# Optimization experiments

Hardware: AMD Instinct MI355X
Metric: run time of the kernel (lower is better)

The kernel has to match this reference:

```python
import jax, jax.numpy as jnp
import numpy as np

N = 100000  # nodes
E = 1600000  # edges


def _gcn_norm(edge_index, num_nodes):
    # PyG GCNConv default: add self-loops, symmetric normalization.
    src, dst = edge_index[0], edge_index[1]
    loop = jnp.arange(num_nodes, dtype=src.dtype)
    src = jnp.concatenate([src, loop])
    dst = jnp.concatenate([dst, loop])
    deg = jax.ops.segment_sum(jnp.ones_like(dst, dtype=jnp.float32), dst,
                              num_segments=num_nodes)
    dinv = jnp.where(deg > 0, jax.lax.rsqrt(deg), 0.0)
    norm = dinv[src] * dinv[dst]  # [E + N]
    return src, dst, norm


def _gcn_layer(x, W, b, src, dst, norm, num_nodes):
    h = x @ W                                # [N, out]
    msg = h[src] * norm[:, None]             # gather + scale, [E+N, out]
    agg = jax.ops.segment_sum(msg, dst, num_segments=num_nodes)
    return agg + b


def setup_inputs() -> dict:
    key = jax.random.key(0)
    ks = jax.random.split(key, 8)
    d_in, d_h, d_out = 128, 128, 64
    x = jax.random.normal(ks[0], (N, d_in), dtype=jnp.float32)
    edge_index = jax.random.randint(ks[1], (2, E), 0, N, dtype=jnp.int64)
    def glorot(k, fan_in, fan_out):
        s = jnp.sqrt(6.0 / (fan_in + fan_out)).astype(jnp.float32)
        return jax.random.uniform(k, (fan_in, fan_out), jnp.float32, -s, s)
    return {
        "x": x,
        "edge_index": edge_index,
        "W1": glorot(ks[2], d_in, d_h), "b1": jnp.zeros((d_h,), jnp.float32),
        "W2": glorot(ks[3], d_h, d_h), "b2": jnp.zeros((d_h,), jnp.float32),
        "W3": glorot(ks[4], d_h, d_out), "b3": jnp.zeros((d_out,), jnp.float32),
    }


def reference(x, edge_index, W1, b1, W2, b2, W3, b3):
    src, dst, norm = _gcn_norm(edge_index, N)
    h = jax.nn.relu(_gcn_layer(x, W1, b1, src, dst, norm, N))
    h = jax.nn.relu(_gcn_layer(h, W2, b2, src, dst, norm, N))
    h = jax.nn.relu(_gcn_layer(h, W3, b3, src, dst, norm, N))
    return h
```

## Files before the change

### kernel.cpp

```cpp
#include <hip/hip_runtime.h>
#include <hip/hip_bf16.h>
#include <hip/hip_fp16.h>


constexpr int N_NODES = 100000;
constexpr int E_EDGES = 1600000;
constexpr int SCAN_B = (N_NODES + 1023) / 1024;

typedef short short8 __attribute__((ext_vector_type(8)));
typedef float f32x4 __attribute__((ext_vector_type(4)));

__global__ __launch_bounds__(256) void count_kernel(
    const int* __restrict__ dst, int* __restrict__ cnt) {
  int e = blockIdx.x * 256 + threadIdx.x;
  if (e < E_EDGES) atomicAdd(&cnt[dst[e]], 1);
}

__global__ __launch_bounds__(256) void scan_part_kernel(
    const int* __restrict__ cnt, int* __restrict__ bsum) {
  __shared__ int red[256];
  const int t = threadIdx.x;
  int base = blockIdx.x * 1024 + t * 4;
  int4 v = make_int4(0, 0, 0, 0);
  if (base < N_NODES) v = *(const int4*)(cnt + base);
  red[t] = v.x + v.y + v.z + v.w;
  __syncthreads();
  for (int off = 128; off > 0; off >>= 1) {
    if (t < off) red[t] += red[t + off];
    __syncthreads();
  }
  if (t == 0) bsum[blockIdx.x] = red[0];
}

__global__ __launch_bounds__(128) void scan_tops_kernel(
    const int* __restrict__ bsum, int* __restrict__ boff,
    int* __restrict__ rowptr) {
  __shared__ int part[128];
  const int t = threadIdx.x;
  int v = (t < SCAN_B) ? bsum[t] : 0;
  part[t] = v;
  __syncthreads();
  for (int off = 1; off < 128; off <<= 1) {
    int add = (t >= off) ? part[t - off] : 0;
    __syncthreads();
    part[t] += add;
    __syncthreads();
  }
  if (t < SCAN_B) boff[t] = part[t] - v;
  if (t == 127) rowptr[N_NODES] = part[127];
}

__global__ __launch_bounds__(256) void scan_write_kernel(
    const int* __restrict__ cnt, const int* __restrict__ boff,
    int* __restrict__ rowptr, float* __restrict__ dinv) {
  __shared__ int part[256];
  const int t = threadIdx.x;
  int base = blockIdx.x * 1024 + t * 4;
  int4 v = make_int4(0, 0, 0, 0);
  if (base < N_NODES) v = *(const int4*)(cnt + base);
  int s = v.x + v.y + v.z + v.w;
  part[t] = s;
  __syncthreads();
  for (int off = 1; off < 256; off <<= 1) {
    int add = (t >= off) ? part[t - off] : 0;
    __syncthreads();
    part[t] += add;
    __syncthreads();
  }
  if (base < N_NODES) {
    int run = boff[blockIdx.x] + part[t] - s;
    int4 o;
    o.x = run;
    o.y = run + v.x;
    o.z = run + v.x + v.y;
    o.w = run + v.x + v.y + v.z;
    *(int4*)(rowptr + base) = o;
    float4 dv;
    dv.x = rsqrtf((float)v.x + 1.0f);
    dv.y = rsqrtf((float)v.y + 1.0f);
    dv.z = rsqrtf((float)v.z + 1.0f);
    dv.w = rsqrtf((float)v.w + 1.0f);
    *(float4*)(dinv + base) = dv;
  }
}

__global__ __launch_bounds__(256) void scatter_kernel(
    const int* __restrict__ src, const int* __restrict__ dst,
    const int* __restrict__ rowptr, int* __restrict__ cursor,
    const float* __restrict__ dinv, int* __restrict__ eSrc,
    float* __restrict__ eW) {
  int e = blockIdx.x * 256 + threadIdx.x;
  if (e < E_EDGES) {
    int s = src[e], d = dst[e];
    int pos = rowptr[d] + atomicAdd(&cursor[d], 1);
    eSrc[pos] = s;
    eW[pos] = dinv[s] * dinv[d];
  }
}

__device__ inline ushort bf_round(float x) {
  uint u = __float_as_uint(x);
  return (ushort)((u + 0x7FFFu + ((u >> 16) & 1u)) >> 16);
}
__device__ inline ushort bf_split(float x, float* rem) {
  ushort h = bf_round(x);
  *rem = x - __uint_as_float((uint)h << 16);
  return h;
}

template <int OC>
__global__ __launch_bounds__(256) void packw_kernel(
    const float* __restrict__ W, ushort* __restrict__ hi,
    ushort* __restrict__ lo) {
  int id = blockIdx.x * 256 + threadIdx.x;
  if (id >= OC * 16) return;
  int col = id & 15;
  int g = (id >> 4) & 3;
  int ks = (id >> 6) & 3;
  int nt = id >> 8;
  int k0 = ks * 32 + g * 8;
  int n = nt * 16 + col;
  ushort h8[8], l8[8];
#pragma unroll
  for (int j = 0; j < 8; ++j) {
    float rem;
    h8[j] = bf_split(W[(size_t)(k0 + j) * OC + n], &rem);
    l8[j] = bf_round(rem);
  }
  size_t base = (size_t)id * 8;
#pragma unroll
  for (int j = 0; j < 8; ++j) {
    hi[base + j] = h8[j];
    lo[base + j] = l8[j];
  }
}

template <int OC>
__global__ __launch_bounds__(256) void gemm_kernel(
    const float* __restrict__ X, const ushort* __restrict__ Whi,
    const ushort* __restrict__ Wlo, __half* __restrict__ H) {
  constexpr int NT = OC / 16;
  __shared__ ushort sWhi[OC * 128];
  __shared__ ushort sWlo[OC * 128];
  const int t = threadIdx.x;
  {
    const uint4* gh = (const uint4*)Whi;
    const uint4* gl = (const uint4*)Wlo;
    uint4* sh = (uint4*)sWhi;
    uint4* sl = (uint4*)sWlo;
    for (int i = t; i < OC * 128 / 8; i += 256) {
      sh[i] = gh[i];
      sl[i] = gl[i];
    }
  }
  const int wid = t >> 6;
  const int lane = t & 63;
  const int row = blockIdx.x * 64 + wid * 16 + (lane & 15);
  const bool ok = row < N_NODES;
  const int g = lane >> 4;

  short8 ahi[4], alo[4];
  const float* xr = X + (size_t)row * 128;
#pragma unroll
  for (int ks = 0; ks < 4; ++ks) {
    float f[8];
    if (ok) {
      float4 f0 = *(const float4*)(xr + ks * 32 + g * 8);
      float4 f1 = *(const float4*)(xr + ks * 32 + g * 8 + 4);
      f[0] = f0.x; f[1] = f0.y; f[2] = f0.z; f[3] = f0.w;
      f[4] = f1.x; f[5] = f1.y; f[6] = f1.z; f[7] = f1.w;
    } else {
#pragma unroll
      for (int j = 0; j < 8; ++j) f[j] = 0.f;
    }
    union { short8 v; ushort u[8]; } h, l;
#pragma unroll
    for (int j = 0; j < 8; ++j) {
      float rem;
      h.u[j] = bf_split(f[j], &rem);
      l.u[j] = bf_round(rem);
    }
    ahi[ks] = h.v;
    alo[ks] = l.v;
  }
  __syncthreads();

#pragma unroll
  for (int nt = 0; nt < NT; ++nt) {
    f32x4 acc = {0.f, 0.f, 0.f, 0.f};
#pragma unroll
    for (int ks = 0; ks < 4; ++ks) {
      int off = (((nt * 4 + ks) * 4 + g) * 16 + (lane & 15)) * 8;
      short8 bhi = *(const short8*)&sWhi[off];
      short8 blo = *(const short8*)&sWlo[off];
      acc = __builtin_amdgcn_mfma_f32_16x16x32_bf16(alo[ks], bhi, acc, 0, 0, 0);
      acc = __builtin_amdgcn_mfma_f32_16x16x32_bf16(ahi[ks], blo, acc, 0, 0, 0);
      acc = __builtin_amdgcn_mfma_f32_16x16x32_bf16(ahi[ks], bhi, acc, 0, 0, 0);
    }
#pragma unroll
    for (int r = 0; r < 4; ++r) {
      int rr = blockIdx.x * 64 + wid * 16 + g * 4 + r;
      if (rr < N_NODES)
        H[(size_t)rr * OC + nt * 16 + (lane & 15)] = __float2half(acc[r]);
    }
  }
}

template <int OC>
__global__ __launch_bounds__(256) void agg_kernel(
    const __half* __restrict__ H, const int* __restrict__ rowptr,
    const int* __restrict__ eSrc, const float* __restrict__ eW,
    const float* __restrict__ dinv, const float* __restrict__ bias,
    float* __restrict__ Y) {
  const int wave = threadIdx.x >> 6;
  const int lane = threadIdx.x & 63;
  const int n = blockIdx.x * 4 + wave;
  if (n >= N_NODES) return;
  const float dn = dinv[n];
  const float selfw = dn * dn;
  const int beg = rowptr[n], end = rowptr[n + 1];
  const int jal = min((beg + 3) & ~3, end);
  const int jend = jal + ((end - jal) & ~7);
  const int jend4 = jend + ((end - jend) & ~3);

  if constexpr (OC == 128) {
    const __half2* H2 = (const __half2*)H;
    float2 hv = __half22float2(H2[(size_t)n * 64 + lane]);
    float ax = hv.x * selfw, ay = hv.y * selfw;
    for (int j = beg; j < jal; ++j) {
      float w = eW[j];
      float2 v = __half22float2(H2[(size_t)eSrc[j] * 64 + lane]);
      ax = fmaf(v.x, w, ax);
      ay = fmaf(v.y, w, ay);
    }
    for (int j = jal; j < jend; j += 8) {
      int4 s0 = *(const int4*)(eSrc + j);
      int4 s1 = *(const int4*)(eSrc + j + 4);
      float4 w0 = *(const float4*)(eW + j);
      float4 w1 = *(const float4*)(eW + j + 4);
      __half2 h0 = H2[(size_t)s0.x * 64 + lane];
      __half2 h1 = H2[(size_t)s0.y * 64 + lane];
      __half2 h2 = H2[(size_t)s0.z * 64 + lane];
      __half2 h3 = H2[(size_t)s0.w * 64 + lane];
      __half2 h4 = H2[(size_t)s1.x * 64 + lane];
      __half2 h5 = H2[(size_t)s1.y * 64 + lane];
      __half2 h6 = H2[(size_t)s1.z * 64 + lane];
      __half2 h7 = H2[(size_t)s1.w * 64 + lane];
      float2 v0 = __half22float2(h0);
      float2 v1 = __half22float2(h1);
      float2 v2 = __half22float2(h2);
      float2 v3 = __half22float2(h3);
      float2 v4 = __half22float2(h4);
      float2 v5 = __half22float2(h5);
      float2 v6 = __half22float2(h6);
      float2 v7 = __half22float2(h7);
      ax = fmaf(v0.x, w0.x, ax); ay = fmaf(v0.y, w0.x, ay);
      ax = fmaf(v1.x, w0.y, ax); ay = fmaf(v1.y, w0.y, ay);
      ax = fmaf(v2.x, w0.z, ax); ay = fmaf(v2.y, w0.z, ay);
      ax = fmaf(v3.x, w0.w, ax); ay = fmaf(v3.y, w0.w, ay);
      ax = fmaf(v4.x, w1.x, ax); ay = fmaf(v4.y, w1.x, ay);
      ax = fmaf(v5.x, w1.y, ax); ay = fmaf(v5.y, w1.y, ay);
      ax = fmaf(v6.x, w1.z, ax); ay = fmaf(v6.y, w1.z, ay);
      ax = fmaf(v7.x, w1.w, ax); ay = fmaf(v7.y, w1.w, ay);
    }
    for (int j = jend; j < jend4; j += 4) {
      int4 s = *(const int4*)(eSrc + j);
      float4 w = *(const float4*)(eW + j);
      float2 v0 = __half22float2(H2[(size_t)s.x * 64 + lane]);
      float2 v1 = __half22float2(H2[(size_t)s.y * 64 + lane]);
      float2 v2 = __half22float2(H2[(size_t)s.z * 64 + lane]);
      float2 v3 = __half22float2(H2[(size_t)s.w * 64 + lane]);
      ax = fmaf(v0.x, w.x, ax); ay = fmaf(v0.y, w.x, ay);
      ax = fmaf(v1.x, w.y, ax); ay = fmaf(v1.y, w.y, ay);
      ax = fmaf(v2.x, w.z, ax); ay = fmaf(v2.y, w.z, ay);
      ax = fmaf(v3.x, w.w, ax); ay = fmaf(v3.y, w.w, ay);
    }
    for (int j = jend4; j < end; ++j) {
      float w = eW[j];
      float2 v = __half22float2(H2[(size_t)eSrc[j] * 64 + lane]);
      ax = fmaf(v.x, w, ax);
      ay = fmaf(v.y, w, ay);
    }
    float2 bb = ((const float2*)bias)[lane];
    float2 o;
    o.x = fmaxf(ax + bb.x, 0.f);
    o.y = fmaxf(ay + bb.y, 0.f);
    ((float2*)Y)[(size_t)n * 64 + lane] = o;
  } else {
    float a = __half2float(H[(size_t)n * 64 + lane]) * selfw;
    for (int j = beg; j < jal; ++j)
      a = fmaf(__half2float(H[(size_t)eSrc[j] * 64 + lane]), eW[j], a);
    for (int j = jal; j < jend; j += 8) {
      int4 s0 = *(const int4*)(eSrc + j);
      int4 s1 = *(const int4*)(eSrc + j + 4);
      float4 w0 = *(const float4*)(eW + j);
      float4 w1 = *(const float4*)(eW + j + 4);
      __half h0 = H[(size_t)s0.x * 64 + lane];
      __half h1 = H[(size_t)s0.y * 64 + lane];
      __half h2 = H[(size_t)s0.z * 64 + lane];
      __half h3 = H[(size_t)s0.w * 64 + lane];
      __half h4 = H[(size_t)s1.x * 64 + lane];
      __half h5 = H[(size_t)s1.y * 64 + lane];
      __half h6 = H[(size_t)s1.z * 64 + lane];
      __half h7 = H[(size_t)s1.w * 64 + lane];
      a = fmaf(__half2float(h0), w0.x, a);
      a = fmaf(__half2float(h1), w0.y, a);
      a = fmaf(__half2float(h2), w0.z, a);
      a = fmaf(__half2float(h3), w0.w, a);
      a = fmaf(__half2float(h4), w1.x, a);
      a = fmaf(__half2float(h5), w1.y, a);
      a = fmaf(__half2float(h6), w1.z, a);
      a = fmaf(__half2float(h7), w1.w, a);
    }
    for (int j = jend; j < jend4; j += 4) {
      int4 s = *(const int4*)(eSrc + j);
      float4 w = *(const float4*)(eW + j);
      a = fmaf(__half2float(H[(size_t)s.x * 64 + lane]), w.x, a);
      a = fmaf(__half2float(H[(size_t)s.y * 64 + lane]), w.y, a);
      a = fmaf(__half2float(H[(size_t)s.z * 64 + lane]), w.z, a);
      a = fmaf(__half2float(H[(size_t)s.w * 64 + lane]), w.w, a);
    }
    for (int j = jend4; j < end; ++j)
      a = fmaf(__half2float(H[(size_t)eSrc[j] * 64 + lane]), eW[j], a);
    Y[(size_t)n * 64 + lane] = fmaxf(a + bias[lane], 0.f);
  }
}

extern "C" void kernel_launch(void* const* d_in, const int* in_sizes, int n_in,
                              void* d_out, int out_size, void* d_ws,
                              size_t ws_size, hipStream_t stream) {
  const float* x = (const float*)d_in[0];
  const int* ei = (const int*)d_in[1];
  const float* W1 = (const float*)d_in[2];
  const float* b1 = (const float*)d_in[3];
  const float* W2 = (const float*)d_in[4];
  const float* b2 = (const float*)d_in[5];
  const float* W3 = (const float*)d_in[6];
  const float* b3 = (const float*)d_in[7];
  const int* src = ei;
  const int* dst = ei + E_EDGES;

  size_t off = 0;
  auto alloc = [&](size_t bytes) -> void* {
    void* p = (char*)d_ws + off;
    off += (bytes + 255) & ~(size_t)255;
    return p;
  };
  int* cnt = (int*)alloc((size_t)N_NODES * 4);
  int* rowptr = (int*)alloc((size_t)(N_NODES + 1) * 4);
  int* cursor = (int*)alloc((size_t)N_NODES * 4);
  float* dinv = (float*)alloc((size_t)N_NODES * 4);
  int* bsum = (int*)alloc((size_t)SCAN_B * 4);
  int* boff = (int*)alloc((size_t)SCAN_B * 4);
  int* eSrc = (int*)alloc((size_t)E_EDGES * 4);
  float* eW = (float*)alloc((size_t)E_EDGES * 4);
  __half* h = (__half*)alloc((size_t)N_NODES * 128 * 2);
  float* A = (float*)alloc((size_t)N_NODES * 128 * 4);
  ushort* wp1h = (ushort*)alloc((size_t)128 * 128 * 2);
  ushort* wp1l = (ushort*)alloc((size_t)128 * 128 * 2);
  ushort* wp2h = (ushort*)alloc((size_t)128 * 128 * 2);
  ushort* wp2l = (ushort*)alloc((size_t)128 * 128 * 2);
  ushort* wp3h = (ushort*)alloc((size_t)128 * 64 * 2);
  ushort* wp3l = (ushort*)alloc((size_t)128 * 64 * 2);

  hipMemsetAsync(cnt, 0, (size_t)N_NODES * 4, stream);
  hipMemsetAsync(cursor, 0, (size_t)N_NODES * 4, stream);

  const int EB = (E_EDGES + 255) / 256;
  count_kernel<<<EB, 256, 0, stream>>>(dst, cnt);
  scan_part_kernel<<<SCAN_B, 256, 0, stream>>>(cnt, bsum);
  scan_tops_kernel<<<1, 128, 0, stream>>>(bsum, boff, rowptr);
  scan_write_kernel<<<SCAN_B, 256, 0, stream>>>(cnt, boff, rowptr, dinv);
  scatter_kernel<<<EB, 256, 0, stream>>>(src, dst, rowptr, cursor, dinv, eSrc,
                                         eW);
  packw_kernel<128><<<8, 256, 0, stream>>>(W1, wp1h, wp1l);
  packw_kernel<128><<<8, 256, 0, stream>>>(W2, wp2h, wp2l);
  packw_kernel<64><<<4, 256, 0, stream>>>(W3, wp3h, wp3l);

  const int GB = (N_NODES + 63) / 64;
  const int AB = (N_NODES + 3) / 4;

  gemm_kernel<128><<<GB, 256, 0, stream>>>(x, wp1h, wp1l, h);
  agg_kernel<128><<<AB, 256, 0, stream>>>(h, rowptr, eSrc, eW, dinv, b1, A);
  gemm_kernel<128><<<GB, 256, 0, stream>>>(A, wp2h, wp2l, h);
  agg_kernel<128><<<AB, 256, 0, stream>>>(h, rowptr, eSrc, eW, dinv, b2, A);
  gemm_kernel<64><<<GB, 256, 0, stream>>>(A, wp3h, wp3l, h);
  agg_kernel<64><<<AB, 256, 0, stream>>>(h, rowptr, eSrc, eW, dinv, b3,
                                         (float*)d_out);
}
```

Before: 437.6 us.

## Interleave CSR source and weight arrays and partition scatter by destination range

Source index and edge weight now sit together in one int2 array, so the aggregation loops need one vector load per pair of edges instead of two separate streams. The scatter kernel now assigns each block to one of 8 destination-node ranges, and each block scans all edges but writes only those in its range. The aim is to localise the cursor atomics and CSR writes into a smaller address window for better cache behaviour. The cost is that every edge's dst is read 8 times.

After: 426.7 us. -2.5%, faster.

```diff
diff --git a/kernel.cpp b/kernel.cpp
--- a/kernel.cpp
+++ b/kernel.cpp
@@ -6,6 +6,8 @@
 constexpr int N_NODES = 100000;
 constexpr int E_EDGES = 1600000;
 constexpr int SCAN_B = (N_NODES + 1023) / 1024;
+constexpr int XGROUPS = 8;
+constexpr int XRANGE = (N_NODES + XGROUPS - 1) / XGROUPS;
 
 typedef short short8 __attribute__((ext_vector_type(8)));
 typedef float f32x4 __attribute__((ext_vector_type(4)));
@@ -87,14 +89,19 @@
 __global__ __launch_bounds__(256) void scatter_kernel(
     const int* __restrict__ src, const int* __restrict__ dst,
     const int* __restrict__ rowptr, int* __restrict__ cursor,
-    const float* __restrict__ dinv, int* __restrict__ eSrc,
-    float* __restrict__ eW) {
-  int e = blockIdx.x * 256 + threadIdx.x;
-  if (e < E_EDGES) {
-    int s = src[e], d = dst[e];
-    int pos = rowptr[d] + atomicAdd(&cursor[d], 1);
-    eSrc[pos] = s;
-    eW[pos] = dinv[s] * dinv[d];
+    const float* __restrict__ dinv, int2* __restrict__ eSW) {
+  const int g = blockIdx.x & 7;
+  const int blk = blockIdx.x >> 3;
+  const int nblk = gridDim.x >> 3;
+  const int lo = g * XRANGE;
+  const int hi = min(lo + XRANGE, N_NODES);
+  for (int e = blk * 256 + threadIdx.x; e < E_EDGES; e += nblk * 256) {
+    int d = dst[e];
+    if (d >= lo && d < hi) {
+      int s = src[e];
+      int pos = rowptr[d] + atomicAdd(&cursor[d], 1);
+      eSW[pos] = make_int2(s, __float_as_int(dinv[s] * dinv[d]));
+    }
   }
 }
 
@@ -209,9 +216,8 @@
 template <int OC>
 __global__ __launch_bounds__(256) void agg_kernel(
     const __half* __restrict__ H, const int* __restrict__ rowptr,
-    const int* __restrict__ eSrc, const float* __restrict__ eW,
-    const float* __restrict__ dinv, const float* __restrict__ bias,
-    float* __restrict__ Y) {
+    const int2* __restrict__ eSW, const float* __restrict__ dinv,
+    const float* __restrict__ bias, float* __restrict__ Y) {
   const int wave = threadIdx.x >> 6;
   const int lane = threadIdx.x & 63;
   const int n = blockIdx.x * 4 + wave;
@@ -219,33 +225,34 @@
   const float dn = dinv[n];
   const float selfw = dn * dn;
   const int beg = rowptr[n], end = rowptr[n + 1];
-  const int jal = min((beg + 3) & ~3, end);
+  const int jal = min(beg + (beg & 1), end);
   const int jend = jal + ((end - jal) & ~7);
-  const int jend4 = jend + ((end - jend) & ~3);
+  const int jend2 = jend + ((end - jend) & ~1);
 
   if constexpr (OC == 128) {
     const __half2* H2 = (const __half2*)H;
     float2 hv = __half22float2(H2[(size_t)n * 64 + lane]);
     float ax = hv.x * selfw, ay = hv.y * selfw;
     for (int j = beg; j < jal; ++j) {
-      float w = eW[j];
-      float2 v = __half22float2(H2[(size_t)eSrc[j] * 64 + lane]);
+      int2 p = eSW[j];
+      float2 v = __half22float2(H2[(size_t)p.x * 64 + lane]);
+      float w = __int_as_float(p.y);
       ax = fmaf(v.x, w, ax);
       ay = fmaf(v.y, w, ay);
     }
     for (int j = jal; j < jend; j += 8) {
-      int4 s0 = *(const int4*)(eSrc + j);
-      int4 s1 = *(const int4*)(eSrc + j + 4);
-      float4 w0 = *(const float4*)(eW + j);
-      float4 w1 = *(const float4*)(eW + j + 4);
-      __half2 h0 = H2[(size_t)s0.x * 64 + lane];
-      __half2 h1 = H2[(size_t)s0.y * 64 + lane];
-      __half2 h2 = H2[(size_t)s0.z * 64 + lane];
-      __half2 h3 = H2[(size_t)s0.w * 64 + lane];
-      __half2 h4 = H2[(size_t)s1.x * 64 + lane];
-      __half2 h5 = H2[(size_t)s1.y * 64 + lane];
-      __half2 h6 = H2[(size_t)s1.z * 64 + lane];
-      __half2 h7 = H2[(size_t)s1.w * 64 + lane];
+      int4 p0 = *(const int4*)(eSW + j);
+      int4 p1 = *(const int4*)(eSW + j + 2);
+      int4 p2 = *(const int4*)(eSW + j + 4);
+      int4 p3 = *(const int4*)(eSW + j + 6);
+      __half2 h0 = H2[(size_t)p0.x * 64 + lane];
+      __half2 h1 = H2[(size_t)p0.z * 64 + lane];
+      __half2 h2 = H2[(size_t)p1.x * 64 + lane];
+      __half2 h3 = H2[(size_t)p1.z * 64 + lane];
+      __half2 h4 = H2[(size_t)p2.x * 64 + lane];
+      __half2 h5 = H2[(size_t)p2.z * 64 + lane];
+      __half2 h6 = H2[(size_t)p3.x * 64 + lane];
+      __half2 h7 = H2[(size_t)p3.z * 64 + lane];
       float2 v0 = __half22float2(h0);
       float2 v1 = __half22float2(h1);
       float2 v2 = __half22float2(h2);
@@ -254,30 +261,36 @@
       float2 v5 = __half22float2(h5);
       float2 v6 = __half22float2(h6);
       float2 v7 = __half22float2(h7);
-      ax = fmaf(v0.x, w0.x, ax); ay = fmaf(v0.y, w0.x, ay);
-      ax = fmaf(v1.x, w0.y, ax); ay = fmaf(v1.y, w0.y, ay);
-      ax = fmaf(v2.x, w0.z, ax); ay = fmaf(v2.y, w0.z, ay);
-      ax = fmaf(v3.x, w0.w, ax); ay = fmaf(v3.y, w0.w, ay);
-      ax = fmaf(v4.x, w1.x, ax); ay = fmaf(v4.y, w1.x, ay);
-      ax = fmaf(v5.x, w1.y, ax); ay = fmaf(v5.y, w1.y, ay);
-      ax = fmaf(v6.x, w1.z, ax); ay = fmaf(v6.y, w1.z, ay);
-      ax = fmaf(v7.x, w1.w, ax); ay = fmaf(v7.y, w1.w, ay);
-    }
-    for (int j = jend; j < jend4; j += 4) {
-      int4 s = *(const int4*)(eSrc + j);
-      float4 w = *(const float4*)(eW + j);
-      float2 v0 = __half22float2(H2[(size_t)s.x * 64 + lane]);
-      float2 v1 = __half22float2(H2[(size_t)s.y * 64 + lane]);
-      float2 v2 = __half22float2(H2[(size_t)s.z * 64 + lane]);
-      float2 v3 = __half22float2(H2[(size_t)s.w * 64 + lane]);
-      ax = fmaf(v0.x, w.x, ax); ay = fmaf(v0.y, w.x, ay);
-      ax = fmaf(v1.x, w.y, ax); ay = fmaf(v1.y, w.y, ay);
-      ax = fmaf(v2.x, w.z, ax); ay = fmaf(v2.y, w.z, ay);
-      ax = fmaf(v3.x, w.w, ax); ay = fmaf(v3.y, w.w, ay);
-    }
-    for (int j = jend4; j < end; ++j) {
-      float w = eW[j];
-      float2 v = __half22float2(H2[(size_t)eSrc[j] * 64 + lane]);
+      ax = fmaf(v0.x, __int_as_float(p0.y), ax);
+      ay = fmaf(v0.y, __int_as_float(p0.y), ay);
+      ax = fmaf(v1.x, __int_as_float(p0.w), ax);
+      ay = fmaf(v1.y, __int_as_float(p0.w), ay);
+      ax = fmaf(v2.x, __int_as_float(p1.y), ax);
+      ay = fmaf(v2.y, __int_as_float(p1.y), ay);
+      ax = fmaf(v3.x, __int_as_float(p1.w), ax);
+      ay = fmaf(v3.y, __int_as_float(p1.w), ay);
+      ax = fmaf(v4.x, __int_as_float(p2.y), ax);
+      ay = fmaf(v4.y, __int_as_float(p2.y), ay);
+      ax = fmaf(v5.x, __int_as_float(p2.w), ax);
+      ay = fmaf(v5.y, __int_as_float(p2.w), ay);
+      ax = fmaf(v6.x, __int_as_float(p3.y), ax);
+      ay = fmaf(v6.y, __int_as_float(p3.y), ay);
+      ax = fmaf(v7.x, __int_as_float(p3.w), ax);
+      ay = fmaf(v7.y, __int_as_float(p3.w), ay);
+    }
+    for (int j = jend; j < jend2; j += 2) {
+      int4 p = *(const int4*)(eSW + j);
+      float2 v0 = __half22float2(H2[(size_t)p.x * 64 + lane]);
+      float2 v1 = __half22float2(H2[(size_t)p.z * 64 + lane]);
+      ax = fmaf(v0.x, __int_as_float(p.y), ax);
+      ay = fmaf(v0.y, __int_as_float(p.y), ay);
+      ax = fmaf(v1.x, __int_as_float(p.w), ax);
+      ay = fmaf(v1.y, __int_as_float(p.w), ay);
+    }
+    for (int j = jend2; j < end; ++j) {
+      int2 p = eSW[j];
+      float2 v = __half22float2(H2[(size_t)p.x * 64 + lane]);
+      float w = __int_as_float(p.y);
       ax = fmaf(v.x, w, ax);
       ay = fmaf(v.y, w, ay);
     }
@@ -288,40 +301,45 @@
     ((float2*)Y)[(size_t)n * 64 + lane] = o;
   } else {
     float a = __half2float(H[(size_t)n * 64 + lane]) * selfw;
-    for (int j = beg; j < jal; ++j)
-      a = fmaf(__half2float(H[(size_t)eSrc[j] * 64 + lane]), eW[j], a);
+    for (int j = beg; j < jal; ++j) {
+      int2 p = eSW[j];
+      a = fmaf(__half2float(H[(size_t)p.x * 64 + lane]),
+               __int_as_float(p.y), a);
+    }
     for (int j = jal; j < jend; j += 8) {
-      int4 s0 = *(const int4*)(eSrc + j);
-      int4 s1 = *(const int4*)(eSrc + j + 4);
-      float4 w0 = *(const float4*)(eW + j);
-      float4 w1 = *(const float4*)(eW + j + 4);
-      __half h0 = H[(size_t)s0.x * 64 + lane];
-      __half h1 = H[(size_t)s0.y * 64 + lane];
-      __half h2 = H[(size_t)s0.z * 64 + lane];
-      __half h3 = H[(size_t)s0.w * 64 + lane];
-      __half h4 = H[(size_t)s1.x * 64 + lane];
-      __half h5 = H[(size_t)s1.y * 64 + lane];
-      __half h6 = H[(size_t)s1.z * 64 + lane];
-      __half h7 = H[(size_t)s1.w * 64 + lane];
-      a = fmaf(__half2float(h0), w0.x, a);
-      a = fmaf(__half2float(h1), w0.y, a);
-      a = fmaf(__half2float(h2), w0.z, a);
-      a = fmaf(__half2float(h3), w0.w, a);
-      a = fmaf(__half2float(h4), w1.x, a);
-      a = fmaf(__half2float(h5), w1.y, a);
-      a = fmaf(__half2float(h6), w1.z, a);
-      a = fmaf(__half2float(h7), w1.w, a);
-    }
-    for (int j = jend; j < jend4; j += 4) {
-      int4 s = *(const int4*)(eSrc + j);
-      float4 w = *(const float4*)(eW + j);
-      a = fmaf(__half2float(H[(size_t)s.x * 64 + lane]), w.x, a);
-      a = fmaf(__half2float(H[(size_t)s.y * 64 + lane]), w.y, a);
-      a = fmaf(__half2float(H[(size_t)s.z * 64 + lane]), w.z, a);
-      a = fmaf(__half2float(H[(size_t)s.w * 64 + lane]), w.w, a);
-    }
-    for (int j = jend4; j < end; ++j)
-      a = fmaf(__half2float(H[(size_t)eSrc[j] * 64 + lane]), eW[j], a);
+      int4 p0 = *(const int4*)(eSW + j);
+      int4 p1 = *(const int4*)(eSW + j + 2);
+      int4 p2 = *(const int4*)(eSW + j + 4);
+      int4 p3 = *(const int4*)(eSW + j + 6);
+      __half h0 = H[(size_t)p0.x * 64 + lane];
+      __half h1 = H[(size_t)p0.z * 64 + lane];
+      __half h2 = H[(size_t)p1.x * 64 + lane];
+      __half h3 = H[(size_t)p1.z * 64 + lane];
+      __half h4 = H[(size_t)p2.x * 64 + lane];
+      __half h5 = H[(size_t)p2.z * 64 + lane];
+      __half h6 = H[(size_t)p3.x * 64 + lane];
+      __half h7 = H[(size_t)p3.z * 64 + lane];
+      a = fmaf(__half2float(h0), __int_as_float(p0.y), a);
+      a = fmaf(__half2float(h1), __int_as_float(p0.w), a);
+      a = fmaf(__half2float(h2), __int_as_float(p1.y), a);
+      a = fmaf(__half2float(h3), __int_as_float(p1.w), a);
+      a = fmaf(__half2float(h4), __int_as_float(p2.y), a);
+      a = fmaf(__half2float(h5), __int_as_float(p2.w), a);
+      a = fmaf(__half2float(h6), __int_as_float(p3.y), a);
+      a = fmaf(__half2float(h7), __int_as_float(p3.w), a);
+    }
+    for (int j = jend; j < jend2; j += 2) {
+      int4 p = *(const int4*)(eSW + j);
+      a = fmaf(__half2float(H[(size_t)p.x * 64 + lane]),
+               __int_as_float(p.y), a);
+      a = fmaf(__half2float(H[(size_t)p.z * 64 + lane]),
+               __int_as_float(p.w), a);
+    }
+    for (int j = jend2; j < end; ++j) {
+      int2 p = eSW[j];
+      a = fmaf(__half2float(H[(size_t)p.x * 64 + lane]),
+               __int_as_float(p.y), a);
+    }
     Y[(size_t)n * 64 + lane] = fmaxf(a + bias[lane], 0.f);
   }
 }
@@ -352,8 +370,7 @@
   float* dinv = (float*)alloc((size_t)N_NODES * 4);
   int* bsum = (int*)alloc((size_t)SCAN_B * 4);
   int* boff = (int*)alloc((size_t)SCAN_B * 4);
-  int* eSrc = (int*)alloc((size_t)E_EDGES * 4);
-  float* eW = (float*)alloc((size_t)E_EDGES * 4);
+  int2* eSW = (int2*)alloc((size_t)E_EDGES * 8);
   __half* h = (__half*)alloc((size_t)N_NODES * 128 * 2);
   float* A = (float*)alloc((size_t)N_NODES * 128 * 4);
   ushort* wp1h = (ushort*)alloc((size_t)128 * 128 * 2);
@@ -371,8 +388,8 @@
   scan_part_kernel<<<SCAN_B, 256, 0, stream>>>(cnt, bsum);
   scan_tops_kernel<<<1, 128, 0, stream>>>(bsum, boff, rowptr);
   scan_write_kernel<<<SCAN_B, 256, 0, stream>>>(cnt, boff, rowptr, dinv);
-  scatter_kernel<<<EB, 256, 0, stream>>>(src, dst, rowptr, cursor, dinv, eSrc,
-                                         eW);
+  scatter_kernel<<<2048, 256, 0, stream>>>(src, dst, rowptr, cursor, dinv,
+                                           eSW);
   packw_kernel<128><<<8, 256, 0, stream>>>(W1, wp1h, wp1l);
   packw_kernel<128><<<8, 256, 0, stream>>>(W2, wp2h, wp2l);
   packw_kernel<64><<<4, 256, 0, stream>>>(W3, wp3h, wp3l);
@@ -381,10 +398,10 @@
   const int AB = (N_NODES + 3) / 4;
 
   gemm_kernel<128><<<GB, 256, 0, stream>>>(x, wp1h, wp1l, h);
-  agg_kernel<128><<<AB, 256, 0, stream>>>(h, rowptr, eSrc, eW, dinv, b1, A);
+  agg_kernel<128><<<AB, 256, 0, stream>>>(h, rowptr, eSW, dinv, b1, A);
   gemm_kernel<128><<<GB, 256, 0, stream>>>(A, wp2h, wp2l, h);
-  agg_kernel<128><<<AB, 256, 0, stream>>>(h, rowptr, eSrc, eW, dinv, b2, A);
+  agg_kernel<128><<<AB, 256, 0, stream>>>(h, rowptr, eSW, dinv, b2, A);
   gemm_kernel<64><<<GB, 256, 0, stream>>>(A, wp3h, wp3l, h);
-  agg_kernel<64><<<AB, 256, 0, stream>>>(h, rowptr, eSrc, eW, dinv, b3,
+  agg_kernel<64><<<AB, 256, 0, stream>>>(h, rowptr, eSW, dinv, b3,
                                          (float*)d_out);
 }
```

## Drop per-edge weight array and compute norms from dinv in aggregation

Applied to the files above, without the earlier changes.

Stops storing a per-edge normalization weight in the scatter pass; each aggregation kernel instead recomputes the weight as dinv[src]*dinv[dst] on the fly. This removes one E-sized write and three E-sized reads of edge weights, at the cost of an extra random gather of dinv per edge in every layer. The count and scatter kernels also process four edges per thread with vectorized nontemporal loads and stores.

Result: slower. 496.4 us (+13.4%).

```diff
diff --git a/kernel.cpp b/kernel.cpp
--- a/kernel.cpp
+++ b/kernel.cpp
@@ -9,11 +9,17 @@
 
 typedef short short8 __attribute__((ext_vector_type(8)));
 typedef float f32x4 __attribute__((ext_vector_type(4)));
+typedef int iv4 __attribute__((ext_vector_type(4)));
 
 __global__ __launch_bounds__(256) void count_kernel(
     const int* __restrict__ dst, int* __restrict__ cnt) {
-  int e = blockIdx.x * 256 + threadIdx.x;
-  if (e < E_EDGES) atomicAdd(&cnt[dst[e]], 1);
+  int i = blockIdx.x * 256 + threadIdx.x;
+  if (i >= E_EDGES / 4) return;
+  iv4 d = __builtin_nontemporal_load((const iv4*)dst + i);
+  atomicAdd(&cnt[d.x], 1);
+  atomicAdd(&cnt[d.y], 1);
+  atomicAdd(&cnt[d.z], 1);
+  atomicAdd(&cnt[d.w], 1);
 }
 
 __global__ __launch_bounds__(256) void scan_part_kernel(
@@ -87,15 +93,19 @@
 __global__ __launch_bounds__(256) void scatter_kernel(
     const int* __restrict__ src, const int* __restrict__ dst,
     const int* __restrict__ rowptr, int* __restrict__ cursor,
-    const float* __restrict__ dinv, int* __restrict__ eSrc,
-    float* __restrict__ eW) {
-  int e = blockIdx.x * 256 + threadIdx.x;
-  if (e < E_EDGES) {
-    int s = src[e], d = dst[e];
-    int pos = rowptr[d] + atomicAdd(&cursor[d], 1);
-    eSrc[pos] = s;
-    eW[pos] = dinv[s] * dinv[d];
-  }
+    int* __restrict__ eSrc) {
+  int i = blockIdx.x * 256 + threadIdx.x;
+  if (i >= E_EDGES / 4) return;
+  iv4 d = __builtin_nontemporal_load((const iv4*)dst + i);
+  iv4 s = __builtin_nontemporal_load((const iv4*)src + i);
+  int p0 = rowptr[d.x] + atomicAdd(&cursor[d.x], 1);
+  int p1 = rowptr[d.y] + atomicAdd(&cursor[d.y], 1);
+  int p2 = rowptr[d.z] + atomicAdd(&cursor[d.z], 1);
+  int p3 = rowptr[d.w] + atomicAdd(&cursor[d.w], 1);
+  __builtin_nontemporal_store(s.x, eSrc + p0);
+  __builtin_nontemporal_store(s.y, eSrc + p1);
+  __builtin_nontemporal_store(s.z, eSrc + p2);
+  __builtin_nontemporal_store(s.w, eSrc + p3);
 }
 
 __device__ inline ushort bf_round(float x) {
@@ -209,9 +219,8 @@
 template <int OC>
 __global__ __launch_bounds__(256) void agg_kernel(
     const __half* __restrict__ H, const int* __restrict__ rowptr,
-    const int* __restrict__ eSrc, const float* __restrict__ eW,
-    const float* __restrict__ dinv, const float* __restrict__ bias,
-    float* __restrict__ Y) {
+    const int* __restrict__ eSrc, const float* __restrict__ dinv,
+    const float* __restrict__ bias, float* __restrict__ Y) {
   const int wave = threadIdx.x >> 6;
   const int lane = threadIdx.x & 63;
   const int n = blockIdx.x * 4 + wave;
@@ -228,16 +237,15 @@
     float2 hv = __half22float2(H2[(size_t)n * 64 + lane]);
     float ax = hv.x * selfw, ay = hv.y * selfw;
     for (int j = beg; j < jal; ++j) {
-      float w = eW[j];
-      float2 v = __half22float2(H2[(size_t)eSrc[j] * 64 + lane]);
+      int s = eSrc[j];
+      float w = dinv[s] * dn;
+      float2 v = __half22float2(H2[(size_t)s * 64 + lane]);
       ax = fmaf(v.x, w, ax);
       ay = fmaf(v.y, w, ay);
     }
     for (int j = jal; j < jend; j += 8) {
       int4 s0 = *(const int4*)(eSrc + j);
       int4 s1 = *(const int4*)(eSrc + j + 4);
-      float4 w0 = *(const float4*)(eW + j);
-      float4 w1 = *(const float4*)(eW + j + 4);
       __half2 h0 = H2[(size_t)s0.x * 64 + lane];
       __half2 h1 = H2[(size_t)s0.y * 64 + lane];
       __half2 h2 = H2[(size_t)s0.z * 64 + lane];
@@ -246,6 +254,14 @@
       __half2 h5 = H2[(size_t)s1.y * 64 + lane];
       __half2 h6 = H2[(size_t)s1.z * 64 + lane];
       __half2 h7 = H2[(size_t)s1.w * 64 + lane];
+      float w0 = dinv[s0.x] * dn;
+      float w1 = dinv[s0.y] * dn;
+      float w2 = dinv[s0.z] * dn;
+      float w3 = dinv[s0.w] * dn;
+      float w4 = dinv[s1.x] * dn;
+      float w5 = dinv[s1.y] * dn;
+      float w6 = dinv[s1.z] * dn;
+      float w7 = dinv[s1.w] * dn;
       float2 v0 = __half22float2(h0);
       float2 v1 = __half22float2(h1);
       float2 v2 = __half22float2(h2);
@@ -254,30 +270,38 @@
       float2 v5 = __half22float2(h5);
       float2 v6 = __half22float2(h6);
       float2 v7 = __half22float2(h7);
-      ax = fmaf(v0.x, w0.x, ax); ay = fmaf(v0.y, w0.x, ay);
-      ax = fmaf(v1.x, w0.y, ax); ay = fmaf(v1.y, w0.y, ay);
-      ax = fmaf(v2.x, w0.z, ax); ay = fmaf(v2.y, w0.z, ay);
-      ax = fmaf(v3.x, w0.w, ax); ay = fmaf(v3.y, w0.w, ay);
-      ax = fmaf(v4.x, w1.x, ax); ay = fmaf(v4.y, w1.x, ay);
-      ax = fmaf(v5.x, w1.y, ax); ay = fmaf(v5.y, w1.y, ay);
-      ax = fmaf(v6.x, w1.z, ax); ay = fmaf(v6.y, w1.z, ay);
-      ax = fmaf(v7.x, w1.w, ax); ay = fmaf(v7.y, w1.w, ay);
+      ax = fmaf(v0.x, w0, ax); ay = fmaf(v0.y, w0, ay);
+      ax = fmaf(v1.x, w1, ax); ay = fmaf(v1.y, w1, ay);
+      ax = fmaf(v2.x, w2, ax); ay = fmaf(v2.y, w2, ay);
+      ax = fmaf(v3.x, w3, ax); ay = fmaf(v3.y, w3, ay);
+      ax = fmaf(v4.x, w4, ax); ay = fmaf(v4.y, w4, ay);
+      ax = fmaf(v5.x, w5, ax); ay = fmaf(v5.y, w5, ay);
+      ax = fmaf(v6.x, w6, ax); ay = fmaf(v6.y, w6, ay);
+      ax = fmaf(v7.x, w7, ax); ay = fmaf(v7.y, w7, ay);
     }
     for (int j = jend; j < jend4; j += 4) {
       int4 s = *(const int4*)(eSrc + j);
-      float4 w = *(const float4*)(eW + j);
-      float2 v0 = __half22float2(H2[(size_t)s.x * 64 + lane]);
-      float2 v1 = __half22float2(H2[(size_t)s.y * 64 + lane]);
-      float2 v2 = __half22float2(H2[(size_t)s.z * 64 + lane]);
-      float2 v3 = __half22float2(H2[(size_t)s.w * 64 + lane]);
-      ax = fmaf(v0.x, w.x, ax); ay = fmaf(v0.y, w.x, ay);
-      ax = fmaf(v1.x, w.y, ax); ay = fmaf(v1.y, w.y, ay);
-      ax = fmaf(v2.x, w.z, ax); ay = fmaf(v2.y, w.z, ay);
-      ax = fmaf(v3.x, w.w, ax); ay = fmaf(v3.y, w.w, ay);
+      __half2 h0 = H2[(size_t)s.x * 64 + lane];
+      __half2 h1 = H2[(size_t)s.y * 64 + lane];
+      __half2 h2 = H2[(size_t)s.z * 64 + lane];
+      __half2 h3 = H2[(size_t)s.w * 64 + lane];
+      float w0 = dinv[s.x] * dn;
+      float w1 = dinv[s.y] * dn;
+      float w2 = dinv[s.z] * dn;
+      float w3 = dinv[s.w] * dn;
+      float2 v0 = __half22float2(h0);
+      float2 v1 = __half22float2(h1);
+      float2 v2 = __half22float2(h2);
+      float2 v3 = __half22float2(h3);
+      ax = fmaf(v0.x, w0, ax); ay = fmaf(v0.y, w0, ay);
+      ax = fmaf(v1.x, w1, ax); ay = fmaf(v1.y, w1, ay);
+      ax = fmaf(v2.x, w2, ax); ay = fmaf(v2.y, w2, ay);
+      ax = fmaf(v3.x, w3, ax); ay = fmaf(v3.y, w3, ay);
     }
     for (int j = jend4; j < end; ++j) {
-      float w = eW[j];
-      float2 v = __half22float2(H2[(size_t)eSrc[j] * 64 + lane]);
+      int s = eSrc[j];
+      float w = dinv[s] * dn;
+      float2 v = __half22float2(H2[(size_t)s * 64 + lane]);
       ax = fmaf(v.x, w, ax);
       ay = fmaf(v.y, w, ay);
     }
@@ -288,13 +312,13 @@
     ((float2*)Y)[(size_t)n * 64 + lane] = o;
   } else {
     float a = __half2float(H[(size_t)n * 64 + lane]) * selfw;
-    for (int j = beg; j < jal; ++j)
-      a = fmaf(__half2float(H[(size_t)eSrc[j] * 64 + lane]), eW[j], a);
+    for (int j = beg; j < jal; ++j) {
+      int s = eSrc[j];
+      a = fmaf(__half2float(H[(size_t)s * 64 + lane]), dinv[s] * dn, a);
+    }
     for (int j = jal; j < jend; j += 8) {
       int4 s0 = *(const int4*)(eSrc + j);
       int4 s1 = *(const int4*)(eSrc + j + 4);
-      float4 w0 = *(const float4*)(eW + j);
-      float4 w1 = *(const float4*)(eW + j + 4);
       __half h0 = H[(size_t)s0.x * 64 + lane];
       __half h1 = H[(size_t)s0.y * 64 + lane];
       __half h2 = H[(size_t)s0.z * 64 + lane];
@@ -303,25 +327,38 @@
       __half h5 = H[(size_t)s1.y * 64 + lane];
       __half h6 = H[(size_t)s1.z * 64 + lane];
       __half h7 = H[(size_t)s1.w * 64 + lane];
-      a = fmaf(__half2float(h0), w0.x, a);
-      a = fmaf(__half2float(h1), w0.y, a);
-      a = fmaf(__half2float(h2), w0.z, a);
-      a = fmaf(__half2float(h3), w0.w, a);
-      a = fmaf(__half2float(h4), w1.x, a);
-      a = fmaf(__half2float(h5), w1.y, a);
-      a = fmaf(__half2float(h6), w1.z, a);
-      a = fmaf(__half2float(h7), w1.w, a);
+      float w0 = dinv[s0.x] * dn;
+      float w1 = dinv[s0.y] * dn;
+      float w2 = dinv[s0.z] * dn;
+      float w3 = dinv[s0.w] * dn;
+      float w4 = dinv[s1.x] * dn;
+      float w5 = dinv[s1.y] * dn;
+      float w6 = dinv[s1.z] * dn;
+      float w7 = dinv[s1.w] * dn;
+      a = fmaf(__half2float(h0), w0, a);
+      a = fmaf(__half2float(h1), w1, a);
+      a = fmaf(__half2float(h2), w2, a);
+      a = fmaf(__half2float(h3), w3, a);
+      a = fmaf(__half2float(h4), w4, a);
+      a = fmaf(__half2float(h5), w5, a);
+      a = fmaf(__half2float(h6), w6, a);
+      a = fmaf(__half2float(h7), w7, a);
     }
     for (int j = jend; j < jend4; j += 4) {
       int4 s = *(const int4*)(eSrc + j);
-      float4 w = *(const float4*)(eW + j);
-      a = fmaf(__half2float(H[(size_t)s.x * 64 + lane]), w.x, a);
-      a = fmaf(__half2float(H[(size_t)s.y * 64 + lane]), w.y, a);
-      a = fmaf(__half2float(H[(size_t)s.z * 64 + lane]), w.z, a);
-      a = fmaf(__half2float(H[(size_t)s.w * 64 + lane]), w.w, a);
-    }
-    for (int j = jend4; j < end; ++j)
-      a = fmaf(__half2float(H[(size_t)eSrc[j] * 64 + lane]), eW[j], a);
+      float w0 = dinv[s.x] * dn;
+      float w1 = dinv[s.y] * dn;
+      float w2 = dinv[s.z] * dn;
+      float w3 = dinv[s.w] * dn;
+      a = fmaf(__half2float(H[(size_t)s.x * 64 + lane]), w0, a);
+      a = fmaf(__half2float(H[(size_t)s.y * 64 + lane]), w1, a);
+      a = fmaf(__half2float(H[(size_t)s.z * 64 + lane]), w2, a);
+      a = fmaf(__half2float(H[(size_t)s.w * 64 + lane]), w3, a);
+    }
+    for (int j = jend4; j < end; ++j) {
+      int s = eSrc[j];
+      a = fmaf(__half2float(H[(size_t)s * 64 + lane]), dinv[s] * dn, a);
+    }
     Y[(size_t)n * 64 + lane] = fmaxf(a + bias[lane], 0.f);
   }
 }
@@ -353,7 +390,6 @@
   int* bsum = (int*)alloc((size_t)SCAN_B * 4);
   int* boff = (int*)alloc((size_t)SCAN_B * 4);
   int* eSrc = (int*)alloc((size_t)E_EDGES * 4);
-  float* eW = (float*)alloc((size_t)E_EDGES * 4);
   __half* h = (__half*)alloc((size_t)N_NODES * 128 * 2);
   float* A = (float*)alloc((size_t)N_NODES * 128 * 4);
   ushort* wp1h = (ushort*)alloc((size_t)128 * 128 * 2);
@@ -366,13 +402,12 @@
   hipMemsetAsync(cnt, 0, (size_t)N_NODES * 4, stream);
   hipMemsetAsync(cursor, 0, (size_t)N_NODES * 4, stream);
 
-  const int EB = (E_EDGES + 255) / 256;
-  count_kernel<<<EB, 256, 0, stream>>>(dst, cnt);
+  const int E4B = (E_EDGES / 4 + 255) / 256;
+  count_kernel<<<E4B, 256, 0, stream>>>(dst, cnt);
   scan_part_kernel<<<SCAN_B, 256, 0, stream>>>(cnt, bsum);
   scan_tops_kernel<<<1, 128, 0, stream>>>(bsum, boff, rowptr);
   scan_write_kernel<<<SCAN_B, 256, 0, stream>>>(cnt, boff, rowptr, dinv);
-  scatter_kernel<<<EB, 256, 0, stream>>>(src, dst, rowptr, cursor, dinv, eSrc,
-                                         eW);
+  scatter_kernel<<<E4B, 256, 0, stream>>>(src, dst, rowptr, cursor, eSrc);
   packw_kernel<128><<<8, 256, 0, stream>>>(W1, wp1h, wp1l);
   packw_kernel<128><<<8, 256, 0, stream>>>(W2, wp2h, wp2l);
   packw_kernel<64><<<4, 256, 0, stream>>>(W3, wp3h, wp3l);
@@ -381,10 +416,10 @@
   const int AB = (N_NODES + 3) / 4;
 
   gemm_kernel<128><<<GB, 256, 0, stream>>>(x, wp1h, wp1l, h);
-  agg_kernel<128><<<AB, 256, 0, stream>>>(h, rowptr, eSrc, eW, dinv, b1, A);
+  agg_kernel<128><<<AB, 256, 0, stream>>>(h, rowptr, eSrc, dinv, b1, A);
   gemm_kernel<128><<<GB, 256, 0, stream>>>(A, wp2h, wp2l, h);
-  agg_kernel<128><<<AB, 256, 0, stream>>>(h, rowptr, eSrc, eW, dinv, b2, A);
+  agg_kernel<128><<<AB, 256, 0, stream>>>(h, rowptr, eSrc, dinv, b2, A);
   gemm_kernel<64><<<GB, 256, 0, stream>>>(A, wp3h, wp3l, h);
-  agg_kernel<64><<<AB, 256, 0, stream>>>(h, rowptr, eSrc, eW, dinv, b3,
+  agg_kernel<64><<<AB, 256, 0, stream>>>(h, rowptr, eSrc, dinv, b3,
                                          (float*)d_out);
 }
```
